# Performance work log

Measured on AMD Instinct MI355X. Metric: run time of the kernel, lower is better.

## Reference

```python
import jax, jax.numpy as jnp
import numpy as np

B, S, E, H, W = 1, 4096, 1024, 16, 256
D = E // H
SCALE = D ** -0.5


def setup_inputs() -> dict:
    key = jax.random.key(0)
    k1, k2, k3 = jax.random.split(key, 3)
    x = jax.random.normal(k1, (B, S, E), dtype=jnp.float32)
    # torch Linear weight is [out,in]; we store transposed [in,out] so y = x @ w
    w_qkv = jax.random.normal(k2, (E, 3 * E), dtype=jnp.float32) * (E ** -0.5)
    w_out = jax.random.normal(k3, (E, E), dtype=jnp.float32) * (E ** -0.5)
    # sliding-window causal mask: key j allowed for query i iff i-W < j <= i
    q_idx = jnp.arange(S)[:, None]
    k_idx = jnp.arange(S)[None, :]
    allowed_mask = (k_idx <= q_idx) & (k_idx > q_idx - W)  # [S,S] bool
    allowed_mask = allowed_mask[None, None]  # [1,1,S,S]
    return {"x": x, "allowed_mask": allowed_mask, "w_qkv": w_qkv, "w_out": w_out}


def reference(x, allowed_mask, w_qkv, w_out):
    b, s, e = x.shape
    qkv = (x @ w_qkv).reshape(b, s, 3, H, D)
    q, k, v = jnp.moveaxis(qkv, 2, 0)  # each [b,s,H,D]
    q = q.transpose(0, 2, 1, 3)  # [b,H,s,D]
    k = k.transpose(0, 2, 1, 3)
    v = v.transpose(0, 2, 1, 3)
    scores = jnp.einsum('bhsd,bhtd->bhst', q, k) * SCALE  # [b,H,s,s]
    scores = jnp.where(allowed_mask, scores, -jnp.inf)
    attn = jax.nn.softmax(scores, axis=-1)
    out = jnp.einsum('bhst,bhtd->bhsd', attn, v)  # [b,H,s,D]
    out = out.transpose(0, 2, 1, 3).reshape(b, s, e)
    return out @ w_out
```

## Files before the change

kernel.cpp:

```cpp
#include <hip/hip_runtime.h>
#include <hip/hip_bf16.h>

#define S_LEN 4096
#define EMB   1024
#define NH    16
#define HD    64
#define WIN   256
#define SCALE 0.125f

typedef __attribute__((ext_vector_type(8))) short short8;
typedef __attribute__((ext_vector_type(4))) float f32x4;
typedef __attribute__((ext_vector_type(4))) unsigned short us4;

__device__ inline unsigned short f2b(float x) {
    __hip_bfloat16 b = __float2bfloat16(x);
    return *reinterpret_cast<unsigned short*>(&b);
}

__device__ inline void gld_lds16(const unsigned short* g, unsigned short* l) {
    __builtin_amdgcn_global_load_lds(
        (const __attribute__((address_space(1))) unsigned int*)g,
        (__attribute__((address_space(3))) unsigned int*)l,
        16, 0, 0);
}

__device__ inline void transpose_tile(const float* __restrict__ in,
                                      unsigned short* __restrict__ out,
                                      int R, int C, int bx, int by,
                                      unsigned short* t) {
    const int tid = threadIdx.x;
    const int r0 = by * 64, c0 = bx * 64;

    const int rr = tid >> 4, cc = (tid & 15) * 4;
    #pragma unroll
    for (int i = 0; i < 4; ++i) {
        float4 v = *reinterpret_cast<const float4*>(&in[(size_t)(r0 + rr + i * 16) * C + c0 + cc]);
        t[(cc + 0) * 72 + rr + i * 16] = f2b(v.x);
        t[(cc + 1) * 72 + rr + i * 16] = f2b(v.y);
        t[(cc + 2) * 72 + rr + i * 16] = f2b(v.z);
        t[(cc + 3) * 72 + rr + i * 16] = f2b(v.w);
    }
    __syncthreads();

    const int wr = tid >> 2, wk = (tid & 3) * 16;
    #pragma unroll
    for (int p = 0; p < 2; ++p)
        *reinterpret_cast<uint4*>(&out[(size_t)(c0 + wr) * R + r0 + wk + p * 8]) =
            *reinterpret_cast<const uint4*>(&t[wr * 72 + wk + p * 8]);
}

__global__ __launch_bounds__(256) void prep(const float* __restrict__ x,
                                            unsigned short* __restrict__ xb,
                                            const float* __restrict__ w_qkv,
                                            unsigned short* __restrict__ wqkvT,
                                            const float* __restrict__ w_out,
                                            unsigned short* __restrict__ woutT) {
    __shared__ alignas(16) unsigned short t[64 * 72];
    const int b = blockIdx.x;
    if (b < 768) {
        transpose_tile(w_qkv, wqkvT, EMB, 3 * EMB, b % 48, b / 48, t);
    } else if (b < 1024) {
        const int bb = b - 768;
        transpose_tile(w_out, woutT, EMB, EMB, bb & 15, bb >> 4, t);
    } else {
        const size_t tt = (size_t)(b - 1024) * 256 + threadIdx.x;
        const float4* s4 = reinterpret_cast<const float4*>(x) + tt * 4;
        float4 v0 = s4[0], v1 = s4[1], v2 = s4[2], v3 = s4[3];
        us4 p0 = {f2b(v0.x), f2b(v0.y), f2b(v0.z), f2b(v0.w)};
        us4 p1 = {f2b(v1.x), f2b(v1.y), f2b(v1.z), f2b(v1.w)};
        us4 p2 = {f2b(v2.x), f2b(v2.y), f2b(v2.z), f2b(v2.w)};
        us4 p3 = {f2b(v3.x), f2b(v3.y), f2b(v3.z), f2b(v3.w)};
        us4* d = reinterpret_cast<us4*>(xb) + tt * 4;
        d[0] = p0; d[1] = p1; d[2] = p2; d[3] = p3;
    }
}

template <int MODE, int BN>
__global__ __launch_bounds__(256) void gemm_bt(const unsigned short* __restrict__ A,
                                               const unsigned short* __restrict__ Bt,
                                               void* __restrict__ Cout,
                                               unsigned short* __restrict__ vT,
                                               int M, int N, int K) {
    constexpr int SMEM_ELEMS = (MODE == 1) ? 17408 : 8192 + BN * 64;
    constexpr int NJ = BN / 32;
    __shared__ alignas(16) unsigned short smem[SMEM_ELEMS];
    unsigned short* As = smem;
    unsigned short* Bs = smem + 8192;

    const int tid  = threadIdx.x;
    const int lane = tid & 63;
    const int w    = tid >> 6;
    const int quad = lane >> 4;
    const int l16  = lane & 15;

    const int m0 = blockIdx.y * 128;
    const int n0 = blockIdx.x * BN;
    const int m_off = (w & 1) * 64;
    const int n_off = (w >> 1) * (BN / 2);

    const int s_row = tid >> 3;
    const int s_c0  = tid & 7;

    f32x4 acc[4][NJ];
    #pragma unroll
    for (int i = 0; i < 4; ++i)
        #pragma unroll
        for (int j = 0; j < NJ; ++j)
            acc[i][j] = (f32x4){0.f, 0.f, 0.f, 0.f};

    for (int bk = 0; bk < K; bk += 64) {
        __syncthreads();
        #pragma unroll
        for (int p = 0; p < 4; ++p) {
            const int row = p * 32 + s_row;
            const int c   = s_c0 ^ (row & 7);
            gld_lds16(A + (size_t)(m0 + row) * K + bk + c * 8,
                      As + (p * 256 + w * 64) * 8);
        }
        #pragma unroll
        for (int p = 0; p < BN / 32; ++p) {
            const int row = p * 32 + s_row;
            const int c   = s_c0 ^ (row & 7);
            gld_lds16(Bt + (size_t)(n0 + row) * K + bk + c * 8,
                      Bs + (p * 256 + w * 64) * 8);
        }
        __syncthreads();

        #pragma unroll
        for (int ks = 0; ks < 2; ++ks) {
            short8 af[4], bf[NJ];
            #pragma unroll
            for (int i = 0; i < 4; ++i) {
                const int r = m_off + i * 16 + l16;
                af[i] = *reinterpret_cast<const short8*>(
                    &As[r * 64 + ((ks * 4 + quad) ^ (r & 7)) * 8]);
            }
            #pragma unroll
            for (int j = 0; j < NJ; ++j) {
                const int r = n_off + j * 16 + l16;
                bf[j] = *reinterpret_cast<const short8*>(
                    &Bs[r * 64 + ((ks * 4 + quad) ^ (r & 7)) * 8]);
            }
            #pragma unroll
            for (int i = 0; i < 4; ++i)
                #pragma unroll
                for (int j = 0; j < NJ; ++j)
                    acc[i][j] = __builtin_amdgcn_mfma_f32_16x16x32_bf16(
                        af[i], bf[j], acc[i][j], 0, 0, 0);
        }
    }

    if (MODE == 0) {
        float* C = (float*)Cout;
        #pragma unroll
        for (int i = 0; i < 4; ++i)
            #pragma unroll
            for (int r = 0; r < 4; ++r) {
                const size_t row = m0 + m_off + i * 16 + quad * 4 + r;
                #pragma unroll
                for (int j = 0; j < NJ; ++j)
                    C[row * N + n0 + n_off + j * 16 + l16] = acc[i][j][r];
            }
    } else if (n0 < 2048) {
        const float sc = (n0 < 1024) ? SCALE : 1.0f;
        unsigned short* C = (unsigned short*)Cout;
        #pragma unroll
        for (int i = 0; i < 4; ++i)
            #pragma unroll
            for (int r = 0; r < 4; ++r) {
                const size_t row = m0 + m_off + i * 16 + quad * 4 + r;
                #pragma unroll
                for (int j = 0; j < NJ; ++j)
                    C[row * N + n0 + n_off + j * 16 + l16] = f2b(acc[i][j][r] * sc);
            }
    } else {
        __syncthreads();
        #pragma unroll
        for (int i = 0; i < 4; ++i) {
            const int ss = m_off + i * 16 + quad * 4;
            #pragma unroll
            for (int j = 0; j < NJ; ++j) {
                const int dd = n_off + j * 16 + l16;
                us4 pk = {f2b(acc[i][j][0]), f2b(acc[i][j][1]),
                          f2b(acc[i][j][2]), f2b(acc[i][j][3])};
                *reinterpret_cast<us4*>(&smem[dd * 136 + ss]) = pk;
            }
        }
        __syncthreads();
        #pragma unroll
        for (int p = 0; p < 8; ++p) {
            const int t  = p * 256 + tid;
            const int dd = t >> 4;
            const int sc2 = (t & 15) * 8;
            *reinterpret_cast<uint4*>(&vT[(size_t)(n0 - 2048 + dd) * S_LEN + m0 + sc2]) =
                *reinterpret_cast<const uint4*>(&smem[dd * 136 + sc2]);
        }
    }
}

__global__ __launch_bounds__(1024, 4) void gemm_qkv(const unsigned short* __restrict__ A,
                                                    const unsigned short* __restrict__ Bt,
                                                    unsigned short* __restrict__ C,
                                                    unsigned short* __restrict__ vT) {
    __shared__ alignas(16) unsigned short smem[65536];

    constexpr int K = EMB;
    const int tid  = threadIdx.x;
    const int lane = tid & 63;
    const int w    = tid >> 6;
    const int quad = lane >> 4;
    const int l16  = lane & 15;
    const int wr   = w >> 2, wc = w & 3;
    const int wm0  = wr * 64, wn0 = wc * 64;

    const int raw = blockIdx.x;
    const int s   = (raw & 7) * 24 + (raw >> 3);
    const int by  = s / 12, bx = s % 12;
    const int m0  = by * 256, n0 = bx * 256;

    const int srow = tid >> 2;
    const int scp  = tid & 3;
    const int sc4  = scp ^ ((srow >> 1) & 3);
    const unsigned short* pA = A  + (size_t)(m0 + srow) * K + sc4 * 8;
    const unsigned short* pB = Bt + (size_t)(n0 + srow) * K + sc4 * 8;
    const int dls = (w * 64) * 8;

    auto STAGE = [&](int q) {
        unsigned short* dA = smem + (q & 3) * 16384 + dls;
        const int gk = q * 32;
        gld_lds16(pA + gk, dA);
        gld_lds16(pB + gk, dA + 8192);
    };

    const int cpf = quad ^ ((l16 >> 1) & 3);
    const int oA  = (wm0 + l16) * 32 + cpf * 8;
    const int oB  = (wn0 + l16) * 32 + cpf * 8;

    f32x4 acc[4][4];
    #pragma unroll
    for (int i = 0; i < 4; ++i)
        #pragma unroll
        for (int j = 0; j < 4; ++j)
            acc[i][j] = (f32x4){0.f, 0.f, 0.f, 0.f};

#define QKV_PH(p, DO_ST, VM) do {                                              \
    const unsigned short* Ab_ = smem + ((p) & 3) * 16384;                      \
    const unsigned short* Bb_ = Ab_ + 8192;                                    \
    short8 af[4], bf[4];                                                       \
    _Pragma("unroll")                                                          \
    for (int i = 0; i < 4; ++i)                                                \
        af[i] = *reinterpret_cast<const short8*>(&Ab_[oA + i * 512]);          \
    _Pragma("unroll")                                                          \
    for (int j = 0; j < 4; ++j)                                                \
        bf[j] = *reinterpret_cast<const short8*>(&Bb_[oB + j * 512]);          \
    if (DO_ST) STAGE((p) + 3);                                                 \
    __builtin_amdgcn_s_setprio(1);                                             \
    _Pragma("unroll")                                                          \
    for (int i = 0; i < 4; ++i)                                                \
        _Pragma("unroll")                                                      \
        for (int j = 0; j < 4; ++j)                                            \
            acc[i][j] = __builtin_amdgcn_mfma_f32_16x16x32_bf16(               \
                af[i], bf[j], acc[i][j], 0, 0, 0);                             \
    __builtin_amdgcn_s_setprio(0);                                             \
    asm volatile("s_waitcnt " VM ::: "memory");                                \
    __builtin_amdgcn_s_barrier();                                              \
} while (0)

    STAGE(0); STAGE(1); STAGE(2);
    asm volatile("s_waitcnt vmcnt(4)" ::: "memory");
    __builtin_amdgcn_s_barrier();

    for (int p = 0; p < 29; ++p)
        QKV_PH(p, true, "vmcnt(4)");
    QKV_PH(29, false, "vmcnt(2)");
    QKV_PH(30, false, "vmcnt(0)");
    QKV_PH(31, false, "vmcnt(0)");
#undef QKV_PH

    const int sec = n0 >> 10;
    if (sec < 2) {
        const float sc = (sec == 0) ? SCALE : 1.0f;
        #pragma unroll
        for (int i = 0; i < 4; ++i) {
            #pragma unroll
            for (int r = 0; r < 4; ++r) {
                const size_t row = (size_t)(m0 + wm0 + i * 16 + quad * 4 + r) * 3072;
                #pragma unroll
                for (int j = 0; j < 4; ++j)
                    C[row + n0 + wn0 + j * 16 + l16] = f2b(acc[i][j][r] * sc);
            }
        }
    } else {
        #pragma unroll
        for (int i = 0; i < 4; ++i) {
            const int ss = wm0 + i * 16 + quad * 4;
            const int sc0 = ss >> 3, se = ss & 7;
            #pragma unroll
            for (int j = 0; j < 4; ++j) {
                const int d = wn0 + j * 16 + l16;
                us4 pk = {f2b(acc[i][j][0]), f2b(acc[i][j][1]),
                          f2b(acc[i][j][2]), f2b(acc[i][j][3])};
                *reinterpret_cast<us4*>(&smem[d * 256 + ((sc0 ^ (d & 31)) << 3) + se]) = pk;
            }
        }
        __builtin_amdgcn_s_barrier();
        const int vb = n0 - 2048;
        #pragma unroll
        for (int rep = 0; rep < 8; ++rep) {
            const int idx = rep * 1024 + tid;
            const int d = idx >> 5, scr = idx & 31;
            *reinterpret_cast<uint4*>(&vT[(size_t)(vb + d) * S_LEN + m0 + scr * 8]) =
                *reinterpret_cast<const uint4*>(&smem[d * 256 + ((scr ^ (d & 31)) << 3)]);
        }
    }
}

typedef __attribute__((ext_vector_type(2))) unsigned int u32x2;

template <int PAR>
__device__ __forceinline__ void pv_phase(const u32x2 (&PA)[17], unsigned short* scrw,
                                         const unsigned short* Vt, f32x4 (&acco)[4],
                                         int ks0, int quad, int l16, short8 af) {
    const int wq  = quad & 1;
    const int tlq = quad >> 1;
    #pragma unroll
    for (int ksi = 0; ksi < 9; ++ksi) {
        if (ksi == 2) { asm volatile("s_waitcnt vmcnt(5)" ::: "memory"); __builtin_amdgcn_s_barrier(); }
        if (ksi == 4) { asm volatile("s_waitcnt vmcnt(3)" ::: "memory"); __builtin_amdgcn_s_barrier(); }
        if (ksi == 6) { asm volatile("s_waitcnt vmcnt(1)" ::: "memory"); __builtin_amdgcn_s_barrier(); }
        if (ksi == 8) { asm volatile("s_waitcnt vmcnt(0)" ::: "memory"); __builtin_amdgcn_s_barrier(); }
        const int ks = ks0 + ksi;
        if (ksi < 8) {
            #pragma unroll
            for (int tl = 0; tl < 2; ++tl) {
                const int nb = 2 * (ksi + 1) + tl - PAR;
                u32x2 v = (nb >= 0 && nb <= 16) ? PA[(nb < 0) ? 0 : ((nb > 16) ? 16 : nb)]
                                                : (u32x2){0u, 0u};
                *reinterpret_cast<u32x2*>(&scrw[((ksi + 1) & 1) * 768 + tl * 384 + l16 * 24 + quad * 4]) = v;
            }
        }
        #pragma unroll
        for (int nb2 = 0; nb2 < 4; ++nb2) {
            const int d = nb2 * 16 + l16;
            const short8 bfr = *reinterpret_cast<const short8*>(
                &Vt[ks * 2048 + d * 32 + ((quad ^ ((d >> 1) & 3)) << 3)]);
            acco[nb2] = __builtin_amdgcn_mfma_f32_16x16x32_bf16(af, bfr, acco[nb2], 0, 0, 0);
        }
        if (ksi < 8)
            af = *reinterpret_cast<const short8*>(&scrw[((ksi + 1) & 1) * 768 + tlq * 384 + l16 * 24 + wq * 8]);
    }
}

__global__ __launch_bounds__(256, 3) void attn_mfma(const unsigned short* __restrict__ qkv,
                                                    const unsigned short* __restrict__ vT,
                                                    unsigned short* __restrict__ outb) {
    __shared__ alignas(16) unsigned short lds[26624];
    unsigned short* KtV = lds;
    unsigned short* scr = lds + 20480;

    const int raw  = blockIdx.x + (blockIdx.y << 6);
    const int xcd  = raw & 7;
    const int slot = raw >> 3;
    const int q0   = (xcd * 8 + (slot & 7)) * 64;
    const int h    = slot >> 3;

    const int tid  = threadIdx.x;
    const int w    = tid >> 6;
    const int lane = tid & 63;
    const int quad = lane >> 4;
    const int l16  = lane & 15;
    const int kbase = q0 - 256;

    const unsigned short* qrow = qkv + (size_t)(q0 + w * 16 + l16) * 3072 + h * 64;
    short8 aq[2];
    aq[0] = *reinterpret_cast<const short8*>(qrow + quad * 8);
    aq[1] = *reinterpret_cast<const short8*>(qrow + 32 + quad * 8);

    #pragma unroll
    for (int i = 0; i < 10; ++i) {
        const int fc  = i * 256 + tid;
        const int row = fc >> 3, p = fc & 7;
        const int c   = p ^ (row & 7);
        int j = kbase + row; if (j < 0) j = 0;
        gld_lds16(qkv + (size_t)j * 3072 + EMB + h * 64 + c * 8,
                  KtV + (i * 256 + w * 64) * 8);
    }

    __syncthreads();

    const int iq = q0 + w * 16 + l16;
    float rsum = 0.f;
    u32x2 PA[17];
    #pragma unroll
    for (int nb = 0; nb < 17; ++nb) {
        const int row = (w + nb) * 16 + l16;
        f32x4 acc = (f32x4){0.f, 0.f, 0.f, 0.f};
        #pragma unroll
        for (int ks = 0; ks < 2; ++ks) {
            const int p = (ks * 4 + quad) ^ (l16 & 7);
            const short8 kf = *reinterpret_cast<const short8*>(&KtV[row * 64 + p * 8]);
            acc = __builtin_amdgcn_mfma_f32_16x16x32_bf16(kf, aq[ks], acc, 0, 0, 0);
        }
        const int jb = kbase + (w + nb) * 16 + quad * 4;
        float ev0, ev1, ev2, ev3;
        {
            const int j0 = jb, j1 = jb + 1, j2 = jb + 2, j3 = jb + 3;
            ev0 = ((j0 >= 0) & (j0 <= iq) & (j0 > iq - WIN)) ? __expf(acc[0]) : 0.f;
            ev1 = ((j1 >= 0) & (j1 <= iq) & (j1 > iq - WIN)) ? __expf(acc[1]) : 0.f;
            ev2 = ((j2 >= 0) & (j2 <= iq) & (j2 > iq - WIN)) ? __expf(acc[2]) : 0.f;
            ev3 = ((j3 >= 0) & (j3 <= iq) & (j3 > iq - WIN)) ? __expf(acc[3]) : 0.f;
        }
        rsum += (ev0 + ev1) + (ev2 + ev3);
        PA[nb][0] = ((unsigned)f2b(ev1) << 16) | f2b(ev0);
        PA[nb][1] = ((unsigned)f2b(ev3) << 16) | f2b(ev2);
    }
    rsum += __shfl_xor(rsum, 16, 64);
    rsum += __shfl_xor(rsum, 32, 64);
    const float inv_l = 1.f / rsum;

    __syncthreads();

    {
        const int vd  = tid >> 2;
        const int vpo = tid & 3;
        const int vsw = vpo ^ ((vd >> 1) & 3);
        const unsigned short* vsrc = vT + (size_t)(h * 64 + vd) * S_LEN;
        #pragma unroll
        for (int i = 0; i < 10; ++i) {
            int j0 = kbase + (4 * i + vsw) * 8; if (j0 < 0) j0 = 0;
            gld_lds16(vsrc + j0, KtV + (i * 256 + w * 64) * 8);
        }
    }

    unsigned short* scrw = scr + w * 1536;
    const int par = w & 1;
    {
        const u32x2 z = {0u, 0u};
        u32x2 v0 = par ? z : PA[0];
        u32x2 v1 = par ? PA[0] : PA[1];
        *reinterpret_cast<u32x2*>(&scrw[0 * 384 + l16 * 24 + quad * 4]) = v0;
        *reinterpret_cast<u32x2*>(&scrw[1 * 384 + l16 * 24 + quad * 4]) = v1;
    }
    const short8 af0 = *reinterpret_cast<const short8*>(
        &scrw[(quad >> 1) * 384 + l16 * 24 + (quad & 1) * 8]);

    asm volatile("s_waitcnt vmcnt(7)" ::: "memory");
    __builtin_amdgcn_s_barrier();

    f32x4 acco[4];
    #pragma unroll
    for (int nb2 = 0; nb2 < 4; ++nb2) acco[nb2] = (f32x4){0.f, 0.f, 0.f, 0.f};

    const int ks0 = w >> 1;
    if (par == 0) pv_phase<0>(PA, scrw, KtV, acco, ks0, quad, l16, af0);
    else          pv_phase<1>(PA, scrw, KtV, acco, ks0, quad, l16, af0);

    float invo[4];
    #pragma unroll
    for (int r = 0; r < 4; ++r)
        invo[r] = __shfl(inv_l, quad * 4 + r, 64);

    #pragma unroll
    for (int nb2 = 0; nb2 < 4; ++nb2)
        #pragma unroll
        for (int r = 0; r < 4; ++r)
            outb[(size_t)(q0 + w * 16 + quad * 4 + r) * EMB + h * 64 + nb2 * 16 + l16] =
                f2b(acco[nb2][r] * invo[r]);
}

extern "C" void kernel_launch(void* const* d_in, const int* in_sizes, int n_in,
                              void* d_out, int out_size, void* d_ws, size_t ws_size,
                              hipStream_t stream) {
    const float* x     = (const float*)d_in[0];
    const float* w_qkv = (const float*)d_in[2];
    const float* w_out = (const float*)d_in[3];
    float* out = (float*)d_out;

    char* ws = (char*)d_ws;
    unsigned short* xb     = (unsigned short*)(ws);
    unsigned short* wqkvT  = (unsigned short*)(ws + (8u  << 20));
    unsigned short* woutT  = (unsigned short*)(ws + (14u << 20));
    unsigned short* qkvb   = (unsigned short*)(ws + (16u << 20));
    unsigned short* attnb  = (unsigned short*)(ws + (48u << 20));
    unsigned short* vT     = (unsigned short*)(ws + (56u << 20));

    prep<<<2048, 256, 0, stream>>>(x, xb, w_qkv, wqkvT, w_out, woutT);

    gemm_qkv<<<dim3(192), 1024, 0, stream>>>(xb, wqkvT, qkvb, vT);

    attn_mfma<<<dim3(S_LEN / 64, NH), 256, 0, stream>>>(qkvb, vT, attnb);

    gemm_bt<0, 64><<<dim3(EMB / 64, S_LEN / 128), 256, 0, stream>>>(
        attnb, woutT, out, nullptr, S_LEN, EMB, EMB);
}
```

Before: 180.6 us.

## Retile QKV GEMM to 256x192 tiles over 256 blocks with double buffering

The QKV projection GEMM moves from 256x256 tiles (192 blocks) to 256x192 tiles (256 blocks), so the grid matches the MI355X's 256 CUs and leaves no second partial wave. The 4-deep LDS pipeline becomes a 2-stage double buffer with a full vmcnt(0) wait each K-step, and LDS use drops from 128KB to 56KB. Because a tile can now straddle the K/V boundary, the epilogue handles each 16-column fragment separately and transposes V in 64-column chunks. This risks exposing more global-load latency, since there is less prefetch depth and a drain every iteration.

After: 182.0 us. Within noise of the previous version (+0.8%).

```diff
diff --git a/kernel.cpp b/kernel.cpp
--- a/kernel.cpp
+++ b/kernel.cpp
@@ -202,7 +202,7 @@
                                                     const unsigned short* __restrict__ Bt,
                                                     unsigned short* __restrict__ C,
                                                     unsigned short* __restrict__ vT) {
-    __shared__ alignas(16) unsigned short smem[65536];
+    __shared__ alignas(16) unsigned short smem[28672];
 
     constexpr int K = EMB;
     const int tid  = threadIdx.x;
@@ -211,106 +211,106 @@
     const int quad = lane >> 4;
     const int l16  = lane & 15;
     const int wr   = w >> 2, wc = w & 3;
-    const int wm0  = wr * 64, wn0 = wc * 64;
+    const int wm0  = wr * 64, wn0 = wc * 48;
 
     const int raw = blockIdx.x;
-    const int s   = (raw & 7) * 24 + (raw >> 3);
-    const int by  = s / 12, bx = s % 12;
-    const int m0  = by * 256, n0 = bx * 256;
-
-    const int srow = tid >> 2;
-    const int scp  = tid & 3;
-    const int sc4  = scp ^ ((srow >> 1) & 3);
-    const unsigned short* pA = A  + (size_t)(m0 + srow) * K + sc4 * 8;
-    const unsigned short* pB = Bt + (size_t)(n0 + srow) * K + sc4 * 8;
-    const int dls = (w * 64) * 8;
+    const int s   = (raw & 7) * 32 + (raw >> 3);
+    const int by  = s >> 4, bx = s & 15;
+    const int m0  = by * 256, n0 = bx * 192;
+
+    const int srowA = tid >> 2;
+    const int scp   = tid & 3;
+    const int scA   = scp ^ ((srowA >> 1) & 3);
+    const int tB    = (tid < 768) ? tid : (tid - 768);
+    const int srowB = tB >> 2;
+    const int scB   = scp ^ ((srowB >> 1) & 3);
+    const unsigned short* pA = A  + (size_t)(m0 + srowA) * K + scA * 8;
+    const unsigned short* pB = Bt + (size_t)(n0 + srowB) * K + scB * 8;
+    const int wB   = (w < 12) ? w : (w - 12);
+    const int dlsA = w * 512;
+    const int dlsB = 8192 + wB * 512;
 
     auto STAGE = [&](int q) {
-        unsigned short* dA = smem + (q & 3) * 16384 + dls;
+        unsigned short* base = smem + (q & 1) * 14336;
         const int gk = q * 32;
-        gld_lds16(pA + gk, dA);
-        gld_lds16(pB + gk, dA + 8192);
+        gld_lds16(pA + gk, base + dlsA);
+        gld_lds16(pB + gk, base + dlsB);
     };
 
     const int cpf = quad ^ ((l16 >> 1) & 3);
     const int oA  = (wm0 + l16) * 32 + cpf * 8;
-    const int oB  = (wn0 + l16) * 32 + cpf * 8;
-
-    f32x4 acc[4][4];
+    const int oB  = 8192 + (wn0 + l16) * 32 + cpf * 8;
+
+    f32x4 acc[4][3];
     #pragma unroll
     for (int i = 0; i < 4; ++i)
         #pragma unroll
-        for (int j = 0; j < 4; ++j)
+        for (int j = 0; j < 3; ++j)
             acc[i][j] = (f32x4){0.f, 0.f, 0.f, 0.f};
 
-#define QKV_PH(p, DO_ST, VM) do {                                              \
-    const unsigned short* Ab_ = smem + ((p) & 3) * 16384;                      \
-    const unsigned short* Bb_ = Ab_ + 8192;                                    \
-    short8 af[4], bf[4];                                                       \
-    _Pragma("unroll")                                                          \
-    for (int i = 0; i < 4; ++i)                                                \
-        af[i] = *reinterpret_cast<const short8*>(&Ab_[oA + i * 512]);          \
-    _Pragma("unroll")                                                          \
-    for (int j = 0; j < 4; ++j)                                                \
-        bf[j] = *reinterpret_cast<const short8*>(&Bb_[oB + j * 512]);          \
-    if (DO_ST) STAGE((p) + 3);                                                 \
-    __builtin_amdgcn_s_setprio(1);                                             \
-    _Pragma("unroll")                                                          \
-    for (int i = 0; i < 4; ++i)                                                \
-        _Pragma("unroll")                                                      \
-        for (int j = 0; j < 4; ++j)                                            \
-            acc[i][j] = __builtin_amdgcn_mfma_f32_16x16x32_bf16(               \
-                af[i], bf[j], acc[i][j], 0, 0, 0);                             \
-    __builtin_amdgcn_s_setprio(0);                                             \
-    asm volatile("s_waitcnt " VM ::: "memory");                                \
-    __builtin_amdgcn_s_barrier();                                              \
-} while (0)
-
-    STAGE(0); STAGE(1); STAGE(2);
-    asm volatile("s_waitcnt vmcnt(4)" ::: "memory");
+    STAGE(0);
+    asm volatile("s_waitcnt vmcnt(0)" ::: "memory");
     __builtin_amdgcn_s_barrier();
 
-    for (int p = 0; p < 29; ++p)
-        QKV_PH(p, true, "vmcnt(4)");
-    QKV_PH(29, false, "vmcnt(2)");
-    QKV_PH(30, false, "vmcnt(0)");
-    QKV_PH(31, false, "vmcnt(0)");
-#undef QKV_PH
-
-    const int sec = n0 >> 10;
-    if (sec < 2) {
-        const float sc = (sec == 0) ? SCALE : 1.0f;
-        #pragma unroll
-        for (int i = 0; i < 4; ++i) {
-            #pragma unroll
-            for (int r = 0; r < 4; ++r) {
-                const size_t row = (size_t)(m0 + wm0 + i * 16 + quad * 4 + r) * 3072;
+    for (int p = 0; p < 32; ++p) {
+        const unsigned short* Rb = smem + (p & 1) * 14336;
+        short8 af[4], bf[3];
+        #pragma unroll
+        for (int i = 0; i < 4; ++i)
+            af[i] = *reinterpret_cast<const short8*>(&Rb[oA + i * 512]);
+        #pragma unroll
+        for (int j = 0; j < 3; ++j)
+            bf[j] = *reinterpret_cast<const short8*>(&Rb[oB + j * 512]);
+        if (p < 31) STAGE(p + 1);
+        __builtin_amdgcn_s_setprio(1);
+        #pragma unroll
+        for (int i = 0; i < 4; ++i)
+            #pragma unroll
+            for (int j = 0; j < 3; ++j)
+                acc[i][j] = __builtin_amdgcn_mfma_f32_16x16x32_bf16(af[i], bf[j], acc[i][j], 0, 0, 0);
+        __builtin_amdgcn_s_setprio(0);
+        asm volatile("s_waitcnt vmcnt(0)" ::: "memory");
+        __builtin_amdgcn_s_barrier();
+    }
+
+    #pragma unroll
+    for (int j = 0; j < 3; ++j) {
+        const int col16 = n0 + wn0 + j * 16;
+        if (col16 < 2048) {
+            const float sc = (col16 < 1024) ? SCALE : 1.0f;
+            #pragma unroll
+            for (int i = 0; i < 4; ++i)
                 #pragma unroll
-                for (int j = 0; j < 4; ++j)
-                    C[row + n0 + wn0 + j * 16 + l16] = f2b(acc[i][j][r] * sc);
-            }
-        }
-    } else {
-        #pragma unroll
-        for (int i = 0; i < 4; ++i) {
-            const int ss = wm0 + i * 16 + quad * 4;
-            const int sc0 = ss >> 3, se = ss & 7;
-            #pragma unroll
-            for (int j = 0; j < 4; ++j) {
-                const int d = wn0 + j * 16 + l16;
-                us4 pk = {f2b(acc[i][j][0]), f2b(acc[i][j][1]),
-                          f2b(acc[i][j][2]), f2b(acc[i][j][3])};
-                *reinterpret_cast<us4*>(&smem[d * 256 + ((sc0 ^ (d & 31)) << 3) + se]) = pk;
-            }
-        }
-        __builtin_amdgcn_s_barrier();
-        const int vb = n0 - 2048;
-        #pragma unroll
-        for (int rep = 0; rep < 8; ++rep) {
-            const int idx = rep * 1024 + tid;
-            const int d = idx >> 5, scr = idx & 31;
-            *reinterpret_cast<uint4*>(&vT[(size_t)(vb + d) * S_LEN + m0 + scr * 8]) =
-                *reinterpret_cast<const uint4*>(&smem[d * 256 + ((scr ^ (d & 31)) << 3)]);
+                for (int r = 0; r < 4; ++r)
+                    C[(size_t)(m0 + wm0 + i * 16 + quad * 4 + r) * 3072 + col16 + l16] =
+                        f2b(acc[i][j][r] * sc);
+        }
+    }
+    if (n0 + 191 >= 2048) {
+        const int vlo = (n0 >= 2048) ? 0 : (2048 - n0);
+        for (int dbase = vlo; dbase < 192; dbase += 64) {
+            __builtin_amdgcn_s_barrier();
+            #pragma unroll
+            for (int j = 0; j < 3; ++j) {
+                const int dcol = wn0 + j * 16;
+                if (dcol >= dbase && dcol < dbase + 64) {
+                    const int dr = dcol - dbase + l16;
+                    #pragma unroll
+                    for (int i = 0; i < 4; ++i) {
+                        us4 pk = {f2b(acc[i][j][0]), f2b(acc[i][j][1]),
+                                  f2b(acc[i][j][2]), f2b(acc[i][j][3])};
+                        *reinterpret_cast<us4*>(&smem[dr * 264 + wm0 + i * 16 + quad * 4]) = pk;
+                    }
+                }
+            }
+            __builtin_amdgcn_s_barrier();
+            #pragma unroll
+            for (int rep = 0; rep < 2; ++rep) {
+                const int idx = rep * 1024 + tid;
+                const int drr = idx >> 5, ch = idx & 31;
+                *reinterpret_cast<uint4*>(&vT[(size_t)(n0 + dbase + drr - 2048) * S_LEN + m0 + ch * 8]) =
+                    *reinterpret_cast<const uint4*>(&smem[drr * 264 + ch * 8]);
+            }
         }
     }
 }
@@ -486,7 +486,7 @@
 
     prep<<<2048, 256, 0, stream>>>(x, xb, w_qkv, wqkvT, w_out, woutT);
 
-    gemm_qkv<<<dim3(192), 1024, 0, stream>>>(xb, wqkvT, qkvb, vT);
+    gemm_qkv<<<dim3(256), 1024, 0, stream>>>(xb, wqkvT, qkvb, vT);
 
     attn_mfma<<<dim3(S_LEN / 64, NH), 256, 0, stream>>>(qkvb, vT, attnb);
 
```
